# Kernel tuning notes

Hardware: AMD Instinct MI355X
Metric: run time of the kernel (lower is better)

## Reference

```python
import jax, jax.numpy as jnp
import numpy as np

THETA = 10000.0
N_HEADS = 16


def setup_inputs() -> dict:
    key = jax.random.key(0)
    kx, kq, kk, kv, ko = jax.random.split(key, 5)
    B, S, D = 2, 2048, 1024
    std = np.sqrt(2.0 / (D + D))
    def mk_w(k):
        # trunc_normal in [-3*std, 3*std], stored as [in_features, out_features]
        return jax.random.truncated_normal(k, -3.0, 3.0, (D, D), jnp.float32) * std
    return {
        "x": jax.random.normal(kx, (B, S, D), dtype=jnp.float32),
        "token_positions": jnp.arange(S, dtype=jnp.int64) if jax.config.jax_enable_x64 else jnp.arange(S, dtype=jnp.int32),
        "WQ": mk_w(kq),
        "WK": mk_w(kk),
        "WV": mk_w(kv),
        "WO": mk_w(ko),
    }


def _rope(x, pos, theta):
    # x: [B, H, S, d_k]; pos: [S]
    d_k = x.shape[-1]
    freq = 1.0 / theta ** (jnp.arange(0, d_k, 2, dtype=jnp.float32) / d_k)  # [d_k//2]
    ang = pos.astype(jnp.float32)[:, None] * freq                            # [S, d_k//2]
    cos, sin = jnp.cos(ang), jnp.sin(ang)
    xp = x.reshape(x.shape[:-1] + (d_k // 2, 2))
    x0, x1 = xp[..., 0], xp[..., 1]
    r0 = cos * x0 - sin * x1
    r1 = sin * x0 + cos * x1
    return jnp.stack([r0, r1], axis=-1).reshape(x.shape)


def reference(x, token_positions, WQ, WK, WV, WO):
    B, S, D = x.shape
    H = N_HEADS
    dk = D // H
    # Linear in source computes y = x @ W.T (W stored [in, out], used transposed)
    def proj(W):
        return jnp.einsum('oi,bsi->bso', W, x).reshape(B, S, H, dk).transpose(0, 2, 1, 3)
    Q = proj(WQ)  # [B, H, S, dk]
    K = proj(WK)
    V = proj(WV)
    Q = _rope(Q, token_positions, THETA)
    K = _rope(K, token_positions, THETA)
    scores = jnp.einsum('bhqd,bhkd->bhqk', Q, K) / np.sqrt(dk).astype(np.float32)
    causal = jnp.tril(jnp.ones((S, S), dtype=bool))
    scores = jnp.where(causal, scores, jnp.float32(-1e9))
    w = jax.nn.softmax(scores, axis=-1)
    out = jnp.einsum('bhqk,bhkd->bhqd', w, V)
    out = out.transpose(0, 2, 1, 3).reshape(B, S, D)
    return jnp.einsum('oi,bsi->bso', WO, out)
```

## Files before the change

### kernel.cpp

```cpp
#include <hip/hip_runtime.h>
#include <hip/hip_bf16.h>

#define S_LEN   2048
#define D_MODEL 1024
#define NH      16
#define DKH     64
#define BATCH   2
#define BS_ROWS 4096

typedef unsigned short u16;
typedef unsigned int   u32;
typedef __attribute__((ext_vector_type(4))) float f32x4;
typedef __attribute__((ext_vector_type(8))) short bf16x8;

__device__ __forceinline__ float bf2f(u16 u) {
  union { unsigned int i; float f; } v; v.i = ((unsigned int)u) << 16; return v.f;
}
__device__ __forceinline__ u16 f2bf(float f) {
  union { __hip_bfloat16 h; u16 u; } cv; cv.h = __float2bfloat16(f); return cv.u;
}
__device__ __forceinline__ f32x4 mfma16(bf16x8 a, bf16x8 b, f32x4 c) {
  return __builtin_amdgcn_mfma_f32_16x16x32_bf16(a, b, c, 0, 0, 0);
}
__device__ __forceinline__ void gl_lds16(const u16* g, u16* l) {
  __builtin_amdgcn_global_load_lds(
      (const __attribute__((address_space(1))) void*)g,
      (__attribute__((address_space(3))) void*)l, 16, 0, 0);
}

__global__ void cvt_all(const float* __restrict__ x,
                        const float* __restrict__ wq, const float* __restrict__ wk,
                        const float* __restrict__ wv, const float* __restrict__ wo,
                        u16* __restrict__ xb, u16* __restrict__ wqb, u16* __restrict__ wkb,
                        u16* __restrict__ wvb, u16* __restrict__ wob) {
  int seg = blockIdx.y;
  const float* src; u16* dst;
  if (seg < 4)      { src = x + (size_t)seg * (1u << 20); dst = xb + (size_t)seg * (1u << 20); }
  else if (seg == 4){ src = wq; dst = wqb; }
  else if (seg == 5){ src = wk; dst = wkb; }
  else if (seg == 6){ src = wv; dst = wvb; }
  else              { src = wo; dst = wob; }
  int i = blockIdx.x * 256 + threadIdx.x;
  float4 v = reinterpret_cast<const float4*>(src)[i];
  ushort4 o;
  o.x = f2bf(v.x); o.y = f2bf(v.y); o.z = f2bf(v.z); o.w = f2bf(v.w);
  reinterpret_cast<ushort4*>(dst)[i] = o;
}

#define BM 128
#define BN 128
#define BKK 64

__global__ __launch_bounds__(256) void gemm_bt(
    const u16* __restrict__ A,
    const u16* __restrict__ B0, const u16* __restrict__ B1, const u16* __restrict__ B2,
    u16* __restrict__ C0, u16* __restrict__ C1, u16* __restrict__ C2,
    float* __restrict__ Cf,
    int M, int N, int K, int out_f32)
{
  __shared__ __align__(16) u16 As[BM * BKK];
  __shared__ __align__(16) u16 Bs[BN * BKK];

  const int z = blockIdx.z;
  const u16* Bm = (z == 0) ? B0 : ((z == 1) ? B1 : B2);
  u16* Cb = (z == 0) ? C0 : ((z == 1) ? C1 : C2);

  const int tid = threadIdx.x;
  const int l = tid & 63, w = tid >> 6;
  const int lr = l & 15, lg = l >> 4;
  const int m0 = blockIdx.y * BM, n0 = blockIdx.x * BN;
  const int wr = w >> 1, wc = w & 1;

  f32x4 acc[4][4];
#pragma unroll
  for (int mi = 0; mi < 4; ++mi)
#pragma unroll
    for (int nj = 0; nj < 4; ++nj)
      acc[mi][nj] = (f32x4){0.f, 0.f, 0.f, 0.f};

  for (int k0 = 0; k0 < K; k0 += BKK) {
    __syncthreads();
#pragma unroll
    for (int i = 0; i < 4; ++i) {
      int Dc = w * 256 + i * 64 + l;
      int row = Dc >> 3;
      int c = (Dc & 7) ^ (row & 7);
      gl_lds16(A  + (size_t)(m0 + row) * K + k0 + c * 8, As + (w * 256 + i * 64) * 8);
      gl_lds16(Bm + (size_t)(n0 + row) * K + k0 + c * 8, Bs + (w * 256 + i * 64) * 8);
    }
    __syncthreads();

    bf16x8 af[2][4], bfr[2][4];
#pragma unroll
    for (int kk = 0; kk < 2; ++kk)
#pragma unroll
      for (int mi = 0; mi < 4; ++mi) {
        int rowa = wr * 64 + mi * 16 + lr;
        int ck = kk * 4 + lg;
        af[kk][mi] = *(const bf16x8*)&As[rowa * BKK + (((ck) ^ (rowa & 7)) << 3)];
        int rowb = wc * 64 + mi * 16 + lr;
        bfr[kk][mi] = *(const bf16x8*)&Bs[rowb * BKK + (((ck) ^ (rowb & 7)) << 3)];
      }
#pragma unroll
    for (int kk = 0; kk < 2; ++kk)
#pragma unroll
      for (int mi = 0; mi < 4; ++mi)
#pragma unroll
        for (int nj = 0; nj < 4; ++nj)
          acc[mi][nj] = mfma16(af[kk][mi], bfr[kk][nj], acc[mi][nj]);
  }

#pragma unroll
  for (int mi = 0; mi < 4; ++mi)
#pragma unroll
    for (int nj = 0; nj < 4; ++nj)
#pragma unroll
      for (int r = 0; r < 4; ++r) {
        int row = m0 + wr * 64 + mi * 16 + lg * 4 + r;
        int col = n0 + wc * 64 + nj * 16 + lr;
        float v = acc[mi][nj][r];
        if (out_f32) Cf[(size_t)row * N + col] = v;
        else         Cb[(size_t)row * N + col] = f2bf(v);
      }
}

__global__ void rope_pack(const u16* __restrict__ Yq, const u16* __restrict__ Yk,
                          const int* __restrict__ pos,
                          u16* __restrict__ Qb, u16* __restrict__ Kb)
{
  int t = blockIdx.x * blockDim.x + threadIdx.x;
  if (t >= BS_ROWS * (D_MODEL / 2)) return;
  int pi = t & 511;
  int r  = t >> 9;
  int h = pi >> 5, j = pi & 31;
  int b = r >> 11, s = r & (S_LEN - 1);
  int p = pos[s];

  float freq = exp2f(-(float)j * 0.41524101186092028f);
  float ang = (float)p * freq;
  float sn, cs;
  sincosf(ang, &sn, &cs);

  int base = r * D_MODEL + pi * 2;
  float q0 = bf2f(Yq[base]), q1 = bf2f(Yq[base + 1]);
  float k0 = bf2f(Yk[base]), k1 = bf2f(Yk[base + 1]);

  const float QS = 0.18033688011112042f;
  float qr0 = (cs * q0 - sn * q1) * QS;
  float qr1 = (sn * q0 + cs * q1) * QS;
  float kr0 = cs * k0 - sn * k1;
  float kr1 = sn * k0 + cs * k1;

  int bh = b * NH + h;
  size_t qidx = ((size_t)bh * S_LEN + s) * DKH + 2 * j;
  ushort2 qo; qo.x = f2bf(qr0); qo.y = f2bf(qr1);
  ushort2 ko; ko.x = f2bf(kr0); ko.y = f2bf(kr1);
  *reinterpret_cast<ushort2*>(Qb + qidx) = qo;
  *reinterpret_cast<ushort2*>(Kb + qidx) = ko;
}

__global__ __launch_bounds__(256) void transpose_v(const u16* __restrict__ Yv,
                                                   u16* __restrict__ Vt)
{
  __shared__ u32 T[64][65];
  const int sb = blockIdx.x;
  const int bh = blockIdx.y;
  const int b = bh >> 4, h = bh & 15;
  const int t = threadIdx.x;
  const int s0 = sb * 64;

#pragma unroll
  for (int pass = 0; pass < 2; ++pass) {
    int row = pass * 32 + (t >> 3);
    int c0 = (t & 7) * 8;
    bf16x8 v = *(const bf16x8*)(Yv + (size_t)(b * S_LEN + s0 + row) * D_MODEL + h * DKH + c0);
#pragma unroll
    for (int i = 0; i < 8; ++i) T[row][c0 + i] = (u32)(u16)v[i];
  }
  __syncthreads();

  const int d = t >> 2, ch = t & 3;
  bf16x8 o0, o1;
#pragma unroll
  for (int i = 0; i < 8; ++i) o0[i] = (short)(u16)T[ch * 16 + i][d];
#pragma unroll
  for (int i = 0; i < 8; ++i) o1[i] = (short)(u16)T[ch * 16 + 8 + i][d];
  u16* dst = Vt + ((size_t)bh * DKH + d) * S_LEN + s0 + ch * 16;
  *(bf16x8*)dst = o0;
  *(bf16x8*)(dst + 8) = o1;
}

__global__ __launch_bounds__(256, 4) void attn_fwd(
    const u16* __restrict__ Qb, const u16* __restrict__ Kb,
    const u16* __restrict__ Vt, u16* __restrict__ Ob)
{
  const int f = blockIdx.x;
  const int qb = 31 - (f >> 5);
  const int bh = f & 31;
  const int b = bh >> 4, h = bh & 15;
  const int tid = threadIdx.x, l = tid & 63, w = tid >> 6;
  const int lr = l & 15, lg = l >> 4;

  __shared__ __align__(16) u16 Ks[2][64 * 64];
  __shared__ __align__(16) u16 Vs[2][64 * 64];
  __shared__ __align__(16) u16 Ps[4][16 * 64];

  const u16* Qh = Qb + (size_t)bh * S_LEN * DKH;
  const u16* Kh = Kb + (size_t)bh * S_LEN * DKH;
  const u16* Vh = Vt + (size_t)bh * DKH * S_LEN;

  const int q0 = qb * 64 + w * 16;

  bf16x8 qf[2];
#pragma unroll
  for (int kk = 0; kk < 2; ++kk)
    qf[kk] = *(const bf16x8*)(Qh + (size_t)(q0 + lr) * DKH + kk * 32 + lg * 8);

  f32x4 oacc[4];
  float m[4], lsum[4];
#pragma unroll
  for (int r = 0; r < 4; ++r) { m[r] = -INFINITY; lsum[r] = 0.f; }
#pragma unroll
  for (int nb = 0; nb < 4; ++nb) oacc[nb] = (f32x4){0.f, 0.f, 0.f, 0.f};

#define STAGE(buf, tt) do {                                                        \
    int kv0s = (tt) * 64;                                                          \
    _Pragma("unroll")                                                              \
    for (int i = 0; i < 2; ++i) {                                                  \
      int Dc = w * 128 + i * 64 + l;                                               \
      int row = Dc >> 3;                                                           \
      int c = (Dc & 7) ^ (row & 7);                                                \
      gl_lds16(Kh + (size_t)(kv0s + row) * DKH + c * 8, &Ks[buf][(w * 128 + i * 64) * 8]); \
      gl_lds16(Vh + (size_t)row * S_LEN + kv0s + c * 8, &Vs[buf][(w * 128 + i * 64) * 8]); \
    }                                                                              \
  } while (0)

  const int nt = qb + 1;
  STAGE(0, 0);
  __syncthreads();
  int cur = 0;
  for (int t = 0; t < nt; ++t) {
    if (t + 1 < nt) STAGE(cur ^ 1, t + 1);
    const int kv0 = t * 64;

    f32x4 sf[4];
#pragma unroll
    for (int nj = 0; nj < 4; ++nj) {
      f32x4 a = (f32x4){0.f, 0.f, 0.f, 0.f};
#pragma unroll
      for (int kk = 0; kk < 2; ++kk) {
        int brow = nj * 16 + lr;
        bf16x8 kf = *(const bf16x8*)&Ks[cur][brow * 64 + (((kk * 4 + lg) ^ (brow & 7)) << 3)];
        a = mfma16(qf[kk], kf, a);
      }
      sf[nj] = a;
    }
    if (t == qb) {
#pragma unroll
      for (int nj = 0; nj < 4; ++nj)
#pragma unroll
        for (int r = 0; r < 4; ++r) {
          int colg = kv0 + nj * 16 + lr;
          int rowg = q0 + lg * 4 + r;
          if (colg > rowg) sf[nj][r] = -1e30f;
        }
    }
    float pm[4];
#pragma unroll
    for (int r = 0; r < 4; ++r) {
      float v = fmaxf(fmaxf(sf[0][r], sf[1][r]), fmaxf(sf[2][r], sf[3][r]));
      v = fmaxf(v, __shfl_xor(v, 1));
      v = fmaxf(v, __shfl_xor(v, 2));
      v = fmaxf(v, __shfl_xor(v, 4));
      v = fmaxf(v, __shfl_xor(v, 8));
      pm[r] = v;
    }
    bool need = false;
#pragma unroll
    for (int r = 0; r < 4; ++r) need = need || (pm[r] > m[r] + 8.f);
    if (__any(need)) {
#pragma unroll
      for (int r = 0; r < 4; ++r) {
        float mn = fmaxf(m[r], pm[r]);
        float sc = exp2f(m[r] - mn);
        m[r] = mn;
        lsum[r] *= sc;
#pragma unroll
        for (int nb = 0; nb < 4; ++nb) oacc[nb][r] *= sc;
      }
    }
    float ps[4] = {0.f, 0.f, 0.f, 0.f};
#pragma unroll
    for (int nj = 0; nj < 4; ++nj)
#pragma unroll
      for (int r = 0; r < 4; ++r) {
        float pv = exp2f(sf[nj][r] - m[r]);
        sf[nj][r] = pv;
        ps[r] += pv;
      }
#pragma unroll
    for (int r = 0; r < 4; ++r) lsum[r] += ps[r];

#pragma unroll
    for (int nj = 0; nj < 4; ++nj)
#pragma unroll
      for (int r = 0; r < 4; ++r) {
        int row = lg * 4 + r, col = nj * 16 + lr;
        int ck = col >> 3;
        Ps[w][row * 64 + ((ck ^ (row & 7)) << 3) + (col & 7)] = f2bf(sf[nj][r]);
      }
#pragma unroll
    for (int kk = 0; kk < 2; ++kk) {
      bf16x8 pa = *(const bf16x8*)&Ps[w][lr * 64 + (((kk * 4 + lg) ^ (lr & 7)) << 3)];
#pragma unroll
      for (int nb = 0; nb < 4; ++nb) {
        int vrow = nb * 16 + lr;
        bf16x8 vf = *(const bf16x8*)&Vs[cur][vrow * 64 + (((kk * 4 + lg) ^ (vrow & 7)) << 3)];
        oacc[nb] = mfma16(pa, vf, oacc[nb]);
      }
    }

    __syncthreads();
    cur ^= 1;
  }
#undef STAGE

  float inv[4];
#pragma unroll
  for (int r = 0; r < 4; ++r) {
    float v = lsum[r];
    v += __shfl_xor(v, 1); v += __shfl_xor(v, 2);
    v += __shfl_xor(v, 4); v += __shfl_xor(v, 8);
    inv[r] = 1.0f / v;
  }
#pragma unroll
  for (int nb = 0; nb < 4; ++nb)
#pragma unroll
    for (int r = 0; r < 4; ++r) {
      int sg = q0 + lg * 4 + r;
      int dg = nb * 16 + lr;
      Ob[(size_t)b * S_LEN * D_MODEL + (size_t)sg * D_MODEL + h * DKH + dg] =
          f2bf(oacc[nb][r] * inv[r]);
    }
}

extern "C" void kernel_launch(void* const* d_in, const int* in_sizes, int n_in,
                              void* d_out, int out_size, void* d_ws, size_t ws_size,
                              hipStream_t stream) {
  const float* x   = (const float*)d_in[0];
  const int*   pos = (const int*)d_in[1];
  const float* WQ  = (const float*)d_in[2];
  const float* WK  = (const float*)d_in[3];
  const float* WV  = (const float*)d_in[4];
  const float* WO  = (const float*)d_in[5];

  char* ws = (char*)d_ws;
  u16* xb  = (u16*)(ws);
  u16* wqb = (u16*)(ws + (size_t)(8)  * 1048576);
  u16* wkb = (u16*)(ws + (size_t)(10) * 1048576);
  u16* wvb = (u16*)(ws + (size_t)(12) * 1048576);
  u16* wob = (u16*)(ws + (size_t)(14) * 1048576);
  u16* Yq  = (u16*)(ws + (size_t)(16) * 1048576);
  u16* Yk  = (u16*)(ws + (size_t)(24) * 1048576);
  u16* Yv  = (u16*)(ws + (size_t)(32) * 1048576);
  u16* Qb  = (u16*)(ws + (size_t)(40) * 1048576);
  u16* Kb  = (u16*)(ws + (size_t)(48) * 1048576);
  u16* Vt  = (u16*)(ws + (size_t)(56) * 1048576);
  u16* Ob  = (u16*)(ws + (size_t)(64) * 1048576);

  cvt_all<<<dim3(1024, 8), 256, 0, stream>>>(x, WQ, WK, WV, WO, xb, wqb, wkb, wvb, wob);

  gemm_bt<<<dim3(D_MODEL / BN, BS_ROWS / BM, 3), 256, 0, stream>>>(
      xb, wqb, wkb, wvb, Yq, Yk, Yv, nullptr, BS_ROWS, D_MODEL, D_MODEL, 0);

  rope_pack<<<(BS_ROWS * (D_MODEL / 2)) / 256, 256, 0, stream>>>(
      Yq, Yk, pos, Qb, Kb);

  transpose_v<<<dim3(S_LEN / 64, BATCH * NH), 256, 0, stream>>>(Yv, Vt);

  attn_fwd<<<dim3(1024), 256, 0, stream>>>(Qb, Kb, Vt, Ob);

  gemm_bt<<<dim3(D_MODEL / BN, BS_ROWS / BM, 1), 256, 0, stream>>>(
      Ob, wob, wob, wob, nullptr, nullptr, nullptr, (float*)d_out,
      BS_ROWS, D_MODEL, D_MODEL, 1);
}
```

Measured before the change: 238.2 us.

## Rewrite attention with 32x32 MFMA, 128-row query tiles and register-resident P

The attention kernel moves from 16x16x32 to 32x32x16 bf16 MFMA. Each block now handles 128 query rows (32 per wave) and computes S transposed so each lane owns one query row, which removes the cross-lane max and sum reductions. P is packed to bf16 in registers and exchanged with lane shuffles instead of going through an LDS round trip. Blocks are reordered to pair long and short causal tiles, and the grid is halved. The trade-off is higher register pressure and lower occupancy (launch bounds 2), plus a per-wave causal skip inside each tile.

```diff
diff --git a/kernel.cpp b/kernel.cpp
--- a/kernel.cpp
+++ b/kernel.cpp
@@ -10,8 +10,9 @@
 
 typedef unsigned short u16;
 typedef unsigned int   u32;
-typedef __attribute__((ext_vector_type(4))) float f32x4;
-typedef __attribute__((ext_vector_type(8))) short bf16x8;
+typedef __attribute__((ext_vector_type(4)))  float f32x4;
+typedef __attribute__((ext_vector_type(16))) float f32x16;
+typedef __attribute__((ext_vector_type(8)))  short bf16x8;
 
 __device__ __forceinline__ float bf2f(u16 u) {
   union { unsigned int i; float f; } v; v.i = ((unsigned int)u) << 16; return v.f;
@@ -19,8 +20,14 @@
 __device__ __forceinline__ u16 f2bf(float f) {
   union { __hip_bfloat16 h; u16 u; } cv; cv.h = __float2bfloat16(f); return cv.u;
 }
+__device__ __forceinline__ u32 pkbf(float a, float b) {
+  return (u32)f2bf(a) | ((u32)f2bf(b) << 16);
+}
 __device__ __forceinline__ f32x4 mfma16(bf16x8 a, bf16x8 b, f32x4 c) {
   return __builtin_amdgcn_mfma_f32_16x16x32_bf16(a, b, c, 0, 0, 0);
+}
+__device__ __forceinline__ f32x16 mfma32(bf16x8 a, bf16x8 b, f32x16 c) {
+  return __builtin_amdgcn_mfma_f32_32x32x16_bf16(a, b, c, 0, 0, 0);
 }
 __device__ __forceinline__ void gl_lds16(const u16* g, u16* l) {
   __builtin_amdgcn_global_load_lds(
@@ -190,38 +197,37 @@
   *(bf16x8*)(dst + 8) = o1;
 }
 
-__global__ __launch_bounds__(256, 4) void attn_fwd(
+__global__ __launch_bounds__(256, 2) void attn_fwd(
     const u16* __restrict__ Qb, const u16* __restrict__ Kb,
     const u16* __restrict__ Vt, u16* __restrict__ Ob)
 {
   const int f = blockIdx.x;
-  const int qb = 31 - (f >> 5);
+  const int qt = (f < 256) ? (f >> 5) : (23 - (f >> 5));
   const int bh = f & 31;
   const int b = bh >> 4, h = bh & 15;
   const int tid = threadIdx.x, l = tid & 63, w = tid >> 6;
-  const int lr = l & 15, lg = l >> 4;
+  const int lq = l & 31;
+  const int hi = l >> 5;
 
   __shared__ __align__(16) u16 Ks[2][64 * 64];
   __shared__ __align__(16) u16 Vs[2][64 * 64];
-  __shared__ __align__(16) u16 Ps[4][16 * 64];
 
   const u16* Qh = Qb + (size_t)bh * S_LEN * DKH;
   const u16* Kh = Kb + (size_t)bh * S_LEN * DKH;
   const u16* Vh = Vt + (size_t)bh * DKH * S_LEN;
 
-  const int q0 = qb * 64 + w * 16;
-
-  bf16x8 qf[2];
-#pragma unroll
-  for (int kk = 0; kk < 2; ++kk)
-    qf[kk] = *(const bf16x8*)(Qh + (size_t)(q0 + lr) * DKH + kk * 32 + lg * 8);
-
-  f32x4 oacc[4];
-  float m[4], lsum[4];
-#pragma unroll
-  for (int r = 0; r < 4; ++r) { m[r] = -INFINITY; lsum[r] = 0.f; }
-#pragma unroll
-  for (int nb = 0; nb < 4; ++nb) oacc[nb] = (f32x4){0.f, 0.f, 0.f, 0.f};
+  const int q0w = qt * 128 + w * 32;
+  const int qg  = q0w + lq;
+
+  bf16x8 qf[4];
+#pragma unroll
+  for (int ks = 0; ks < 4; ++ks)
+    qf[ks] = *(const bf16x8*)(Qh + (size_t)qg * DKH + ks * 16 + hi * 8);
+
+  f32x16 oacc[2];
+#pragma unroll
+  for (int r = 0; r < 16; ++r) { oacc[0][r] = 0.f; oacc[1][r] = 0.f; }
+  float m = -INFINITY, lsum = 0.f;
 
 #define STAGE(buf, tt) do {                                                        \
     int kv0s = (tt) * 64;                                                          \
@@ -235,113 +241,106 @@
     }                                                                              \
   } while (0)
 
-  const int nt = qb + 1;
+  const int nt = 2 * qt + 2;
   STAGE(0, 0);
   __syncthreads();
   int cur = 0;
   for (int t = 0; t < nt; ++t) {
     if (t + 1 < nt) STAGE(cur ^ 1, t + 1);
     const int kv0 = t * 64;
-
-    f32x4 sf[4];
-#pragma unroll
-    for (int nj = 0; nj < 4; ++nj) {
-      f32x4 a = (f32x4){0.f, 0.f, 0.f, 0.f};
-#pragma unroll
-      for (int kk = 0; kk < 2; ++kk) {
-        int brow = nj * 16 + lr;
-        bf16x8 kf = *(const bf16x8*)&Ks[cur][brow * 64 + (((kk * 4 + lg) ^ (brow & 7)) << 3)];
-        a = mfma16(qf[kk], kf, a);
-      }
-      sf[nj] = a;
+    if (kv0 <= q0w + 31) {
+      f32x16 sv0, sv1;
+#pragma unroll
+      for (int r = 0; r < 16; ++r) { sv0[r] = 0.f; sv1[r] = 0.f; }
+#pragma unroll
+      for (int ks = 0; ks < 4; ++ks) {
+        int c0 = ((ks * 2 + hi) ^ (l & 7)) << 3;
+        bf16x8 k0 = *(const bf16x8*)&Ks[cur][lq * 64 + c0];
+        bf16x8 k1 = *(const bf16x8*)&Ks[cur][(32 + lq) * 64 + c0];
+        sv0 = mfma32(k0, qf[ks], sv0);
+        sv1 = mfma32(k1, qf[ks], sv1);
+      }
+      if (kv0 + 63 > q0w) {
+#pragma unroll
+        for (int r = 0; r < 16; ++r) {
+          int kvl = (r & 3) + 8 * (r >> 2) + 4 * hi;
+          if (kv0 + kvl > qg)      sv0[r] = -1e30f;
+          if (kv0 + 32 + kvl > qg) sv1[r] = -1e30f;
+        }
+      }
+      float pm = sv0[0];
+#pragma unroll
+      for (int r = 1; r < 16; ++r) pm = fmaxf(pm, sv0[r]);
+#pragma unroll
+      for (int r = 0; r < 16; ++r) pm = fmaxf(pm, sv1[r]);
+      pm = fmaxf(pm, __shfl_xor(pm, 32));
+      if (__any(pm > m + 8.f)) {
+        float mn = fmaxf(m, pm);
+        float sc = exp2f(m - mn);
+        m = mn; lsum *= sc;
+#pragma unroll
+        for (int r = 0; r < 16; ++r) {
+          float sr = __shfl(sc, (r & 3) + 8 * (r >> 2) + 4 * hi);
+          oacc[0][r] *= sr; oacc[1][r] *= sr;
+        }
+      }
+      float ps = 0.f;
+#pragma unroll
+      for (int r = 0; r < 16; ++r) { float p = exp2f(sv0[r] - m); sv0[r] = p; ps += p; }
+#pragma unroll
+      for (int r = 0; r < 16; ++r) { float p = exp2f(sv1[r] - m); sv1[r] = p; ps += p; }
+      lsum += ps;
+#pragma unroll
+      for (int s = 0; s < 2; ++s) {
+        u32 w0[4], w1[4];
+#pragma unroll
+        for (int g = 0; g < 4; ++g) {
+          float a0 = s ? sv1[4 * g]     : sv0[4 * g];
+          float a1 = s ? sv1[4 * g + 1] : sv0[4 * g + 1];
+          float a2 = s ? sv1[4 * g + 2] : sv0[4 * g + 2];
+          float a3 = s ? sv1[4 * g + 3] : sv0[4 * g + 3];
+          w0[g] = pkbf(a0, a1);
+          w1[g] = pkbf(a2, a3);
+        }
+#pragma unroll
+        for (int t2 = 0; t2 < 2; ++t2) {
+          u32 xo0 = hi ? w0[2 * t2 + 1] : w0[2 * t2];
+          u32 xo1 = hi ? w1[2 * t2 + 1] : w1[2 * t2];
+          u32 sp0 = hi ? w0[2 * t2]     : w0[2 * t2 + 1];
+          u32 sp1 = hi ? w1[2 * t2]     : w1[2 * t2 + 1];
+          u32 yo0 = __shfl_xor(sp0, 32);
+          u32 yo1 = __shfl_xor(sp1, 32);
+          union { u32 u[4]; bf16x8 v; } pa;
+          pa.u[0] = hi ? yo0 : xo0;
+          pa.u[1] = hi ? yo1 : xo1;
+          pa.u[2] = hi ? xo0 : yo0;
+          pa.u[3] = hi ? xo1 : yo1;
+          int ks2 = s * 2 + t2;
+          int cv = ((ks2 * 2 + hi) ^ (l & 7)) << 3;
+#pragma unroll
+          for (int dh = 0; dh < 2; ++dh) {
+            bf16x8 vf = *(const bf16x8*)&Vs[cur][(dh * 32 + lq) * 64 + cv];
+            oacc[dh] = mfma32(pa.v, vf, oacc[dh]);
+          }
+        }
+      }
     }
-    if (t == qb) {
-#pragma unroll
-      for (int nj = 0; nj < 4; ++nj)
-#pragma unroll
-        for (int r = 0; r < 4; ++r) {
-          int colg = kv0 + nj * 16 + lr;
-          int rowg = q0 + lg * 4 + r;
-          if (colg > rowg) sf[nj][r] = -1e30f;
-        }
-    }
-    float pm[4];
-#pragma unroll
-    for (int r = 0; r < 4; ++r) {
-      float v = fmaxf(fmaxf(sf[0][r], sf[1][r]), fmaxf(sf[2][r], sf[3][r]));
-      v = fmaxf(v, __shfl_xor(v, 1));
-      v = fmaxf(v, __shfl_xor(v, 2));
-      v = fmaxf(v, __shfl_xor(v, 4));
-      v = fmaxf(v, __shfl_xor(v, 8));
-      pm[r] = v;
-    }
-    bool need = false;
-#pragma unroll
-    for (int r = 0; r < 4; ++r) need = need || (pm[r] > m[r] + 8.f);
-    if (__any(need)) {
-#pragma unroll
-      for (int r = 0; r < 4; ++r) {
-        float mn = fmaxf(m[r], pm[r]);
-        float sc = exp2f(m[r] - mn);
-        m[r] = mn;
-        lsum[r] *= sc;
-#pragma unroll
-        for (int nb = 0; nb < 4; ++nb) oacc[nb][r] *= sc;
-      }
-    }
-    float ps[4] = {0.f, 0.f, 0.f, 0.f};
-#pragma unroll
-    for (int nj = 0; nj < 4; ++nj)
-#pragma unroll
-      for (int r = 0; r < 4; ++r) {
-        float pv = exp2f(sf[nj][r] - m[r]);
-        sf[nj][r] = pv;
-        ps[r] += pv;
-      }
-#pragma unroll
-    for (int r = 0; r < 4; ++r) lsum[r] += ps[r];
-
-#pragma unroll
-    for (int nj = 0; nj < 4; ++nj)
-#pragma unroll
-      for (int r = 0; r < 4; ++r) {
-        int row = lg * 4 + r, col = nj * 16 + lr;
-        int ck = col >> 3;
-        Ps[w][row * 64 + ((ck ^ (row & 7)) << 3) + (col & 7)] = f2bf(sf[nj][r]);
-      }
-#pragma unroll
-    for (int kk = 0; kk < 2; ++kk) {
-      bf16x8 pa = *(const bf16x8*)&Ps[w][lr * 64 + (((kk * 4 + lg) ^ (lr & 7)) << 3)];
-#pragma unroll
-      for (int nb = 0; nb < 4; ++nb) {
-        int vrow = nb * 16 + lr;
-        bf16x8 vf = *(const bf16x8*)&Vs[cur][vrow * 64 + (((kk * 4 + lg) ^ (vrow & 7)) << 3)];
-        oacc[nb] = mfma16(pa, vf, oacc[nb]);
-      }
-    }
-
     __syncthreads();
     cur ^= 1;
   }
 #undef STAGE
 
-  float inv[4];
-#pragma unroll
-  for (int r = 0; r < 4; ++r) {
-    float v = lsum[r];
-    v += __shfl_xor(v, 1); v += __shfl_xor(v, 2);
-    v += __shfl_xor(v, 4); v += __shfl_xor(v, 8);
-    inv[r] = 1.0f / v;
+  float ltot = lsum + __shfl_xor(lsum, 32);
+  float inv = 1.0f / ltot;
+  u16* obase = Ob + (size_t)b * S_LEN * D_MODEL + (size_t)h * DKH;
+#pragma unroll
+  for (int r = 0; r < 16; ++r) {
+    int ql = (r & 3) + 8 * (r >> 2) + 4 * hi;
+    float ir = __shfl(inv, ql);
+    u16* orow = obase + (size_t)(q0w + ql) * D_MODEL;
+    orow[lq]      = f2bf(oacc[0][r] * ir);
+    orow[32 + lq] = f2bf(oacc[1][r] * ir);
   }
-#pragma unroll
-  for (int nb = 0; nb < 4; ++nb)
-#pragma unroll
-    for (int r = 0; r < 4; ++r) {
-      int sg = q0 + lg * 4 + r;
-      int dg = nb * 16 + lr;
-      Ob[(size_t)b * S_LEN * D_MODEL + (size_t)sg * D_MODEL + h * DKH + dg] =
-          f2bf(oacc[nb][r] * inv[r]);
-    }
 }
 
 extern "C" void kernel_launch(void* const* d_in, const int* in_sizes, int n_in,
@@ -378,7 +377,7 @@
 
   transpose_v<<<dim3(S_LEN / 64, BATCH * NH), 256, 0, stream>>>(Yv, Vt);
 
-  attn_fwd<<<dim3(1024), 256, 0, stream>>>(Qb, Kb, Vt, Ob);
+  attn_fwd<<<dim3(512), 256, 0, stream>>>(Qb, Kb, Vt, Ob);
 
   gemm_bt<<<dim3(D_MODEL / BN, BS_ROWS / BM, 1), 256, 0, stream>>>(
       Ob, wob, wob, wob, nullptr, nullptr, nullptr, (float*)d_out,
```

After: 226.9 us. 1.05x faster.
